# Optimization experiments

Hardware: AMD Instinct MI355X
Metric: run time of the kernel (lower is better)

## Reference

```python
import jax, jax.numpy as jnp
import numpy as np

BETA = 0.25


def setup_inputs() -> dict:
    key = jax.random.key(0)
    k1, k2 = jax.random.split(key)
    n_e, dim_e = 1024, 256
    z = jax.random.normal(k1, (32, dim_e, 32, 32), dtype=jnp.float32)
    # nn.Embedding init: uniform(-1/n_e, 1/n_e)
    embeddings = jax.random.uniform(k2, (n_e, dim_e), dtype=jnp.float32,
                                    minval=-1.0 / n_e, maxval=1.0 / n_e)
    return {"z": z, "embeddings": embeddings}


def reference(z, embeddings):
    B, C, H, W = z.shape
    # (B,C,H,W) -> (B*H*W, C)
    z_flat = jnp.transpose(z, (0, 2, 3, 1)).reshape(-1, C)
    # squared L2 distances to every codebook vector: (N, n_e)
    distances = (jnp.sum(z_flat ** 2, axis=1, keepdims=True)
                 + jnp.sum(embeddings ** 2, axis=1)
                 - 2.0 * z_flat @ embeddings.T)
    idx = jnp.argmin(distances, axis=1)  # (N,)
    # quantized vectors, back to (B,C,H,W)
    z_q = embeddings[idx].reshape(B, H, W, C).transpose(0, 3, 1, 2)
    sg = jax.lax.stop_gradient
    loss = (jnp.mean((sg(z_q) - z) ** 2)
            + BETA * jnp.mean((z_q - sg(z)) ** 2))
    # module returns the index map (B,H,W) and the scalar loss
    return idx.reshape(B, H, W), loss
```

## Files before the change

### kernel.cpp

```cpp
#include <hip/hip_runtime.h>


#define NE   1024
#define DIM  256
#define BHW  32768
#define CST  1024
#define BST  262144
#define NTH  256
#define MT   128
#define NT   128
#define KT   16
#define RT   8
#define CTY  8
#define ZSTR 160
#define NKT  (DIM / KT)
#define GAP_MFMA 1.5e-4f
#define GAP_F32  2.5e-4f

#define OFF_SUME   0
#define OFF_LOSS   4096
#define OFF_CNT    4112
#define OFF_T1     8192
#define OFF_BESTD  139264
#define OFF_LIST   270336
#define OFF_EMBT   401408
#define OFF_PART1  1449984
#define OFF_PART2  3547136
#define OFF_ZA     5242880
#define OFF_EB     38797312
#define WS_FAST_NEED 40894464ull

typedef unsigned long long ull;
typedef __attribute__((ext_vector_type(8))) short bf16x8;
typedef __attribute__((ext_vector_type(4))) float f32x4;

__device__ __forceinline__ unsigned short bf16rne(float x) {
    unsigned u = __float_as_uint(x);
    return (unsigned short)((u + 0x7fffu + ((u >> 16) & 1u)) >> 16);
}

__device__ __forceinline__ void gll16(const void* g, void* l) {
    __builtin_amdgcn_global_load_lds(
        (const __attribute__((address_space(1))) unsigned int*)g,
        (__attribute__((address_space(3))) unsigned int*)l, 16, 0, 0);
}

__device__ __forceinline__ float keyhi(ull k) {
    return __uint_as_float((unsigned)(k >> 32));
}
__device__ __forceinline__ void kmerge(ull& m1, float& m2, ull x1, float x2) {
    if (x1 < m1) { m2 = fminf(x2, keyhi(m1)); m1 = x1; }
    else          m2 = fminf(m2, keyhi(x1));
}

__device__ __forceinline__ float np_pw128_sq_contig(const float* p) {
    float r[8];
#pragma unroll
    for (int k = 0; k < 8; ++k) r[k] = __fmul_rn(p[k], p[k]);
    for (int i = 8; i < 128; i += 8) {
#pragma unroll
        for (int k = 0; k < 8; ++k)
            r[k] = __fadd_rn(r[k], __fmul_rn(p[i + k], p[i + k]));
    }
    return __fadd_rn(__fadd_rn(__fadd_rn(r[0], r[1]), __fadd_rn(r[2], r[3])),
                     __fadd_rn(__fadd_rn(r[4], r[5]), __fadd_rn(r[6], r[7])));
}

__global__ __launch_bounds__(NTH) void vq_prep(const float* __restrict__ emb,
                                               const float* __restrict__ z,
                                               float* __restrict__ sume,
                                               float* __restrict__ embT,
                                               unsigned short* __restrict__ Eb,
                                               unsigned short* __restrict__ Za,
                                               float* __restrict__ t1,
                                               double* __restrict__ loss_acc,
                                               int* __restrict__ cnt,
                                               int doEb) {
    __shared__ float zt[256 * 66];
    const int tid = threadIdx.x;

    if (blockIdx.x < 128) {
        if (blockIdx.x == 0 && tid == 0) { *loss_acc = 0.0; *cnt = 0; }
        const int j0   = blockIdx.x * 8;
        const int jloc = tid >> 5;
        const int c0   = (tid & 31) * 8;
        const int j    = j0 + jloc;

        const float4* gp = (const float4*)(emb + (size_t)j * DIM + c0);
        float4 v0 = gp[0], v1 = gp[1];
        float v[8] = {v0.x, v0.y, v0.z, v0.w, v1.x, v1.y, v1.z, v1.w};

#pragma unroll
        for (int k = 0; k < 8; ++k) zt[jloc * 264 + c0 + k] = v[k];

        if (doEb) {
            bf16x8 p1, p2;
#pragma unroll
            for (int k = 0; k < 8; ++k) {
                unsigned short b1 = bf16rne(v[k]);
                float b1f = __uint_as_float((unsigned)b1 << 16);
                unsigned short b2 = bf16rne(__fsub_rn(v[k], b1f));
                p1[k] = (short)b1;
                p2[k] = (short)b2;
            }
            const int kta = c0 >> 5, pos = c0 & 31;
            *(bf16x8*)(Eb + (size_t)kta * 32768 + (size_t)j * 32 + pos)       = p1;
            *(bf16x8*)(Eb + (size_t)(kta + 8) * 32768 + (size_t)j * 32 + pos) = p2;
        }
        __syncthreads();
        {
            float col[8];
#pragma unroll
            for (int r = 0; r < 8; ++r) col[r] = zt[r * 264 + tid];
            float4 w0 = {col[0], col[1], col[2], col[3]};
            float4 w1 = {col[4], col[5], col[6], col[7]};
            *(float4*)(embT + (size_t)tid * NE + j0)     = w0;
            *(float4*)(embT + (size_t)tid * NE + j0 + 4) = w1;
        }
        if (tid < 8) {
            const float* p = &zt[tid * 264];
            sume[j0 + tid] = __fadd_rn(np_pw128_sq_contig(p),
                                       np_pw128_sq_contig(p + 128));
        }
        return;
    }

    const int zb = blockIdx.x - 128;
    const int b = zb >> 4, hw0 = (zb & 15) * 64;
    const int idx = tid & 63, cq = tid >> 6;
    for (int c = cq * 64; c < cq * 64 + 64; ++c)
        zt[c * 66 + idx] = z[(size_t)b * BST + (size_t)c * CST + hw0 + idx];
    __syncthreads();
    if (tid < 64) {
        float r[8], h[2];
#pragma unroll
        for (int half = 0; half < 2; ++half) {
            int c0 = half * 128;
#pragma unroll
            for (int k = 0; k < 8; ++k) {
                float v = zt[(c0 + k) * 66 + tid];
                r[k] = __fmul_rn(v, v);
            }
            for (int c = 8; c < 128; ++c) {
                float v = zt[(c0 + c) * 66 + tid];
                r[c & 7] = __fadd_rn(r[c & 7], __fmul_rn(v, v));
            }
            h[half] = __fadd_rn(
                __fadd_rn(__fadd_rn(r[0], r[1]), __fadd_rn(r[2], r[3])),
                __fadd_rn(__fadd_rn(r[4], r[5]), __fadd_rn(r[6], r[7])));
        }
        t1[b * 1024 + hw0 + tid] = __fadd_rn(h[0], h[1]);
    }
    const int l = tid & 63, seg = tid >> 6;
    const int rloc = seg * 16 + (l >> 2), piece = l & 3;
    const int n = b * 1024 + hw0 + rloc;
    for (int kt = 0; kt < 16; ++kt) {
        bf16x8 pack;
        int cbase = (kt & 7) * 32 + piece * 8;
#pragma unroll
        for (int jj = 0; jj < 8; ++jj) {
            float zf = zt[(cbase + jj) * 66 + rloc];
            unsigned short a1 = bf16rne(zf);
            unsigned short v = a1;
            if (kt >= 8) {
                float a1f = __uint_as_float((unsigned)a1 << 16);
                v = bf16rne(__fsub_rn(zf, a1f));
            }
            pack[jj] = (short)v;
        }
        *(bf16x8*)(Za + (size_t)kt * 1048576 + (size_t)n * 32 + piece * 8) = pack;
    }
}

__global__ __launch_bounds__(NTH) void vq_mfma(const unsigned short* __restrict__ Za,
                                               const unsigned short* __restrict__ Eb,
                                               const float* __restrict__ sume,
                                               const float* __restrict__ t1g,
                                               ull* __restrict__ part1,
                                               float* __restrict__ part2) {
    __shared__ __align__(16) unsigned short As[8192];
    __shared__ __align__(16) unsigned short Bs[8192];
    __shared__ ull   red1[128];
    __shared__ float red2[128];

    const int tid = threadIdx.x;
    const int w = tid >> 6, lane = tid & 63;
    const int wr = w & 1, wc = w >> 1;
    const int c15 = lane & 15, q = lane >> 4;
    const int blk = blockIdx.x;
    const int ct = (blk >> 3) & 7;
    const int rowtile = ((blk >> 6) << 3) | (blk & 7);
    const int row0 = rowtile * MT;

    const int perm = (lane >> 2) * 32 + (((lane & 3) ^ ((lane >> 3) & 3)) * 8);
    const int qs = (q ^ ((c15 >> 1) & 3)) * 8;

    f32x4 acc[4][4];
#pragma unroll
    for (int i = 0; i < 4; ++i)
#pragma unroll
        for (int jb = 0; jb < 4; ++jb) acc[i][jb] = (f32x4){0.f, 0.f, 0.f, 0.f};

    const int s0 = w * 2;
    for (int ktp = 0; ktp < 8; ++ktp) {
        __syncthreads();
        {
            const unsigned short* gAlo = Za + (size_t)ktp * 1048576 + (size_t)row0 * 32;
            const unsigned short* gAhi = gAlo + 8u * 1048576u;
            const unsigned short* gBlo = Eb + (size_t)ktp * 32768 + (size_t)ct * 4096;
            const unsigned short* gBhi = gBlo + 8u * 32768u;
#pragma unroll
            for (int ss = 0; ss < 2; ++ss) {
                const int s = s0 + ss;
                gll16(gAlo + s * 512 + perm, (void*)&As[s * 512]);
                gll16(gAhi + s * 512 + perm, (void*)&As[4096 + s * 512]);
                gll16(gBlo + s * 512 + perm, (void*)&Bs[s * 512]);
                gll16(gBhi + s * 512 + perm, (void*)&Bs[4096 + s * 512]);
            }
        }
        __syncthreads();

        bf16x8 bl[4], bh[4];
#pragma unroll
        for (int jb = 0; jb < 4; ++jb) {
            const int nn = (wc * 64 + jb * 16 + c15) * 32 + qs;
            bl[jb] = *(const bf16x8*)&Bs[nn];
            bh[jb] = *(const bf16x8*)&Bs[4096 + nn];
        }
#pragma unroll
        for (int i = 0; i < 4; ++i) {
            const int mm = (wr * 64 + i * 16 + c15) * 32 + qs;
            bf16x8 al = *(const bf16x8*)&As[mm];
            bf16x8 ah = *(const bf16x8*)&As[4096 + mm];
#pragma unroll
            for (int jb = 0; jb < 4; ++jb) {
                acc[i][jb] = __builtin_amdgcn_mfma_f32_16x16x32_bf16(
                    al, bl[jb], acc[i][jb], 0, 0, 0);
                acc[i][jb] = __builtin_amdgcn_mfma_f32_16x16x32_bf16(
                    al, bh[jb], acc[i][jb], 0, 0, 0);
                acc[i][jb] = __builtin_amdgcn_mfma_f32_16x16x32_bf16(
                    ah, bl[jb], acc[i][jb], 0, 0, 0);
            }
        }
    }

    float sme[4];
#pragma unroll
    for (int jb = 0; jb < 4; ++jb)
        sme[jb] = sume[ct * 128 + wc * 64 + jb * 16 + c15];

    ull   mm1[4][4];
    float mm2[4][4];
#pragma unroll
    for (int i = 0; i < 4; ++i) {
#pragma unroll
        for (int reg = 0; reg < 4; ++reg) {
            int row = row0 + wr * 64 + i * 16 + q * 4 + reg;
            float t1v = t1g[row];
            ull m1 = ~0ull;
            float m2 = 3.4e38f;
#pragma unroll
            for (int jb = 0; jb < 4; ++jb) {
                float d = __fsub_rn(__fadd_rn(t1v, sme[jb]),
                                    __fmul_rn(2.0f, acc[i][jb][reg]));
                ull key = ((ull)__float_as_uint(d) << 32) |
                          (unsigned)(ct * 128 + wc * 64 + jb * 16 + c15);
                kmerge(m1, m2, key, 3.4e38f);
            }
#pragma unroll
            for (int m = 1; m < 16; m <<= 1) {
                ull x1 = __shfl_xor(m1, m);
                float x2 = __shfl_xor(m2, m);
                kmerge(m1, m2, x1, x2);
            }
            mm1[i][reg] = m1;
            mm2[i][reg] = m2;
        }
    }
    if (wc == 0 && c15 == 0) {
#pragma unroll
        for (int i = 0; i < 4; ++i)
#pragma unroll
            for (int reg = 0; reg < 4; ++reg) {
                red1[wr * 64 + i * 16 + q * 4 + reg] = mm1[i][reg];
                red2[wr * 64 + i * 16 + q * 4 + reg] = mm2[i][reg];
            }
    }
    __syncthreads();
    if (wc == 1 && c15 == 0) {
#pragma unroll
        for (int i = 0; i < 4; ++i)
#pragma unroll
            for (int reg = 0; reg < 4; ++reg) {
                int loc = wr * 64 + i * 16 + q * 4 + reg;
                ull m1 = mm1[i][reg];
                float m2 = mm2[i][reg];
                kmerge(m1, m2, red1[loc], red2[loc]);
                part1[(size_t)ct * BHW + row0 + loc] = m1;
                part2[(size_t)ct * BHW + row0 + loc] = m2;
            }
    }
}

__global__ __launch_bounds__(NTH) void vq_main_f32(const float* __restrict__ z,
                                                   const float* __restrict__ emb,
                                                   const float* __restrict__ sume,
                                                   const float* __restrict__ t1g,
                                                   ull* __restrict__ part1,
                                                   float* __restrict__ part2) {
    __shared__ __align__(16) char smem[25344];
    float* zs = (float*)smem;
    float* es = zs + KT * ZSTR;
    ull* red1 = (ull*)smem;
    float* red2 = (float*)(smem + 16896);

    const int tid = threadIdx.x;
    const int rowtile = blockIdx.x & 255;
    const int split = blockIdx.x >> 8;
    const int row0 = rowtile * MT;
    const int b = row0 >> 10;
    const int hw0 = row0 & 1023;
    const int rg = tid & 15, cg = tid >> 4;
    const int sm = tid & 127, skh = tid >> 7;
    const int sn = tid >> 1, skq = tid & 1;

    const float* zstg = z + (size_t)b * BST + hw0 + sm;
    const int zi = (sm >> 3) * 10 + (sm & 7);
    const int ei = (sn >> 3) * 10 + (sn & 7);

    float t1v[RT];
#pragma unroll
    for (int i = 0; i < RT; ++i) t1v[i] = t1g[row0 + rg * RT + i];

    ull b1[RT];
    float b2[RT];
#pragma unroll
    for (int i = 0; i < RT; ++i) { b1[i] = ~0ull; b2[i] = 3.4e38f; }

    const int code0 = split * NT;
    float accf[RT][CTY];
#pragma unroll
    for (int i = 0; i < RT; ++i)
#pragma unroll
        for (int j = 0; j < CTY; ++j) accf[i][j] = 0.0f;

    float smv[CTY];
#pragma unroll
    for (int j = 0; j < CTY; ++j) smv[j] = sume[code0 + cg * CTY + j];

    const float* estg = emb + (size_t)(code0 + sn) * DIM + skq * 8;

    for (int kt = 0; kt < NKT; ++kt) {
        __syncthreads();
        {
            const float* zp = zstg + (size_t)(kt * KT + skh) * CST;
#pragma unroll
            for (int kk = 0; kk < 8; ++kk)
                zs[(kk * 2 + skh) * ZSTR + zi] = zp[(size_t)(kk * 2) * CST];
        }
        {
            const float4* ep = (const float4*)(estg + kt * KT);
            float4 e0 = ep[0], e1 = ep[1];
            float ev[8] = {e0.x, e0.y, e0.z, e0.w, e1.x, e1.y, e1.z, e1.w};
#pragma unroll
            for (int qq = 0; qq < 8; ++qq)
                es[(skq * 8 + qq) * ZSTR + ei] = ev[qq];
        }
        __syncthreads();

#pragma unroll 2
        for (int k = 0; k < KT; ++k) {
            const float* zf = &zs[k * ZSTR + rg * 10];
            const float* ef = &es[k * ZSTR + cg * 10];
            float zr[RT], er[CTY];
#pragma unroll
            for (int i = 0; i < RT; ++i) zr[i] = zf[i];
#pragma unroll
            for (int j = 0; j < CTY; ++j) er[j] = ef[j];
#pragma unroll
            for (int i = 0; i < RT; ++i)
#pragma unroll
                for (int j = 0; j < CTY; ++j)
                    accf[i][j] = fmaf(zr[i], er[j], accf[i][j]);
        }
    }

#pragma unroll
    for (int i = 0; i < RT; ++i)
#pragma unroll
        for (int j = 0; j < CTY; ++j) {
            float d = __fsub_rn(__fadd_rn(t1v[i], smv[j]),
                                __fmul_rn(2.0f, accf[i][j]));
            ull key = ((ull)__float_as_uint(d) << 32) |
                      (unsigned)(code0 + cg * CTY + j);
            kmerge(b1[i], b2[i], key, 3.4e38f);
        }

    __syncthreads();
#pragma unroll
    for (int i = 0; i < RT; ++i) {
        red1[cg * 132 + rg * RT + i] = b1[i];
        red2[cg * 132 + rg * RT + i] = b2[i];
    }
    __syncthreads();
    if (tid < MT) {
        ull m1 = red1[tid];
        float m2 = red2[tid];
#pragma unroll
        for (int c = 1; c < 16; ++c)
            kmerge(m1, m2, red1[c * 132 + tid], red2[c * 132 + tid]);
        part1[(size_t)split * BHW + row0 + tid] = m1;
        part2[(size_t)split * BHW + row0 + tid] = m2;
    }
}

__global__ __launch_bounds__(NTH) void vq_t1(const float* __restrict__ z,
                                             float* __restrict__ t1) {
    int n = blockIdx.x * NTH + threadIdx.x;
    int b = n >> 10, hw = n & 1023;
    const float* p = z + (size_t)b * BST + hw;
    float r[8], h[2];
#pragma unroll
    for (int half = 0; half < 2; ++half) {
        int c0 = half * 128;
#pragma unroll
        for (int k = 0; k < 8; ++k) {
            float v = p[(size_t)(c0 + k) * CST];
            r[k] = __fmul_rn(v, v);
        }
        for (int c = 8; c < 128; ++c) {
            float v = p[(size_t)(c0 + c) * CST];
            r[c & 7] = __fadd_rn(r[c & 7], __fmul_rn(v, v));
        }
        h[half] = __fadd_rn(
            __fadd_rn(__fadd_rn(r[0], r[1]), __fadd_rn(r[2], r[3])),
            __fadd_rn(__fadd_rn(r[4], r[5]), __fadd_rn(r[6], r[7])));
    }
    t1[n] = __fadd_rn(h[0], h[1]);
}

__global__ __launch_bounds__(NTH) void vq_combine(const ull* __restrict__ part1,
                                                  const float* __restrict__ part2,
                                                  float* __restrict__ out,
                                                  float* __restrict__ bestd,
                                                  int* __restrict__ list,
                                                  int* __restrict__ cnt,
                                                  double* __restrict__ loss_acc,
                                                  float gapthr) {
    __shared__ double sdd[NTH];
    const int n = blockIdx.x * NTH + threadIdx.x;
    ull m1 = part1[n];
    float m2 = part2[n];
    for (int s = 1; s < 8; ++s)
        kmerge(m1, m2, part1[(size_t)s * BHW + n], part2[(size_t)s * BHW + n]);
    int j = (int)(m1 & 0xffffffffu);
    float d1 = keyhi(m1);
    out[n] = (float)j;
    bestd[n] = d1;
    float gap = __fsub_rn(m2, d1);
    if (!(gap >= gapthr)) {
        int p = atomicAdd(cnt, 1);
        list[p] = n;
    }
    sdd[threadIdx.x] = (double)d1;
    __syncthreads();
    for (int s = NTH / 2; s > 0; s >>= 1) {
        if (threadIdx.x < s) sdd[threadIdx.x] += sdd[threadIdx.x + s];
        __syncthreads();
    }
    if (threadIdx.x == 0) atomicAdd(loss_acc, sdd[0]);
}

__global__ __launch_bounds__(NTH) void vq_recheck(const float* __restrict__ z,
                                                  const float* __restrict__ embT,
                                                  const float* __restrict__ sume,
                                                  const float* __restrict__ t1g,
                                                  const int* __restrict__ list,
                                                  const int* __restrict__ cnt,
                                                  float* __restrict__ out,
                                                  const float* __restrict__ bestd,
                                                  double* __restrict__ loss_acc) {
    __shared__ float zs[DIM];
    __shared__ ull sk[NTH];
    const int t = threadIdx.x;
    int count = *cnt;
    if (count > BHW) count = BHW;
    const float4* ev = (const float4*)embT;

    for (int li = blockIdx.x; li < count; li += gridDim.x) {
        const int n = list[li];
        const int bb = n >> 10, hw = n & 1023;
        __syncthreads();
        zs[t] = z[(size_t)bb * BST + (size_t)t * CST + hw];
        __syncthreads();

        double acc[4] = {0.0, 0.0, 0.0, 0.0};
#pragma unroll 4
        for (int c = 0; c < DIM; ++c) {
            float4 e = ev[c * 256 + t];
            double zv = (double)zs[c];
            acc[0] = fma(zv, (double)e.x, acc[0]);
            acc[1] = fma(zv, (double)e.y, acc[1]);
            acc[2] = fma(zv, (double)e.z, acc[2]);
            acc[3] = fma(zv, (double)e.w, acc[3]);
        }
        const float t1v = t1g[n];
        const float4 sm = ((const float4*)sume)[t];
        const float smv[4] = {sm.x, sm.y, sm.z, sm.w};
        ull bk = ~0ull;
#pragma unroll
        for (int jj = 0; jj < 4; ++jj) {
            int j = t * 4 + jj;
            float d = __fsub_rn(__fadd_rn(t1v, smv[jj]),
                                __fmul_rn(2.0f, (float)acc[jj]));
            ull key = ((ull)__float_as_uint(d) << 32) | (unsigned)j;
            if (key < bk) bk = key;
        }
        sk[t] = bk;
        __syncthreads();
        for (int s = NTH / 2; s > 0; s >>= 1) {
            if (t < s) { ull o = sk[t + s]; if (o < sk[t]) sk[t] = o; }
            __syncthreads();
        }
        if (t == 0) {
            int j = (int)(sk[0] & 0xffffffffu);
            out[n] = (float)j;
            atomicAdd(loss_acc, (double)keyhi(sk[0]) - (double)bestd[n]);
        }
    }
}

__global__ void vq_final(const double* __restrict__ acc,
                         float* __restrict__ out) {
    double m = *acc / 8388608.0;
    float mf = (float)m;
    out[BHW] = __fadd_rn(mf, __fmul_rn(0.25f, mf));
}

extern "C" void kernel_launch(void* const* d_in, const int* in_sizes, int n_in,
                              void* d_out, int out_size, void* d_ws, size_t ws_size,
                              hipStream_t stream) {
    const float* z = (const float*)d_in[0];
    const float* emb = (const float*)d_in[1];
    float* out = (float*)d_out;

    char* ws = (char*)d_ws;
    float* sume = (float*)(ws + OFF_SUME);
    double* loss_acc = (double*)(ws + OFF_LOSS);
    int* cnt = (int*)(ws + OFF_CNT);
    float* t1 = (float*)(ws + OFF_T1);
    float* bestd = (float*)(ws + OFF_BESTD);
    int* list = (int*)(ws + OFF_LIST);
    float* embT = (float*)(ws + OFF_EMBT);
    ull* part1 = (ull*)(ws + OFF_PART1);
    float* part2 = (float*)(ws + OFF_PART2);
    unsigned short* Za = (unsigned short*)(ws + OFF_ZA);
    unsigned short* Eb = (unsigned short*)(ws + OFF_EB);

    const bool fast = ws_size >= WS_FAST_NEED;

    if (fast) {
        vq_prep<<<640, NTH, 0, stream>>>(emb, z, sume, embT, Eb, Za, t1,
                                         loss_acc, cnt, 1);
        vq_mfma<<<2048, NTH, 0, stream>>>(Za, Eb, sume, t1, part1, part2);
    } else {
        vq_prep<<<128, NTH, 0, stream>>>(emb, z, sume, embT, Eb, Za, t1,
                                         loss_acc, cnt, 0);
        vq_t1<<<BHW / NTH, NTH, 0, stream>>>(z, t1);
        vq_main_f32<<<2048, NTH, 0, stream>>>(z, emb, sume, t1, part1, part2);
    }
    vq_combine<<<BHW / NTH, NTH, 0, stream>>>(part1, part2, out, bestd, list, cnt,
                                              loss_acc, fast ? GAP_MFMA : GAP_F32);
    vq_recheck<<<2048, NTH, 0, stream>>>(z, embT, sume, t1, list, cnt, out, bestd,
                                         loss_acc);
    vq_final<<<1, 1, 0, stream>>>(loss_acc, out);
}
```

Baseline: 219.5 us.

## Fuse combine, recheck and final loss into one post kernel

Merges the partial-result combine, the fp64 recheck of near-tie rows and the final loss reduction into a single kernel. Each block keeps its ambiguous rows in a shared-memory list and rechecks them locally. A last-block-done counter then writes the scalar loss. This removes two kernel launches, the global candidate list and the bestd round-trip. The cost is that rechecks run serially within each of 128 blocks rather than across a 2048-block grid, which could create imbalance if many rows are ambiguous.

Measured after the change: 378.3 us. 1.72x slower.

```diff
diff --git a/kernel.cpp b/kernel.cpp
--- a/kernel.cpp
+++ b/kernel.cpp
@@ -19,10 +19,8 @@
 
 #define OFF_SUME   0
 #define OFF_LOSS   4096
-#define OFF_CNT    4112
+#define OFF_DONE   4112
 #define OFF_T1     8192
-#define OFF_BESTD  139264
-#define OFF_LIST   270336
 #define OFF_EMBT   401408
 #define OFF_PART1  1449984
 #define OFF_PART2  3547136
@@ -74,13 +72,13 @@
                                                unsigned short* __restrict__ Za,
                                                float* __restrict__ t1,
                                                double* __restrict__ loss_acc,
-                                               int* __restrict__ cnt,
+                                               int* __restrict__ done,
                                                int doEb) {
     __shared__ float zt[256 * 66];
     const int tid = threadIdx.x;
 
     if (blockIdx.x < 128) {
-        if (blockIdx.x == 0 && tid == 0) { *loss_acc = 0.0; *cnt = 0; }
+        if (blockIdx.x == 0 && tid == 0) { *loss_acc = 0.0; *done = 0; }
         const int j0   = blockIdx.x * 8;
         const int jloc = tid >> 5;
         const int c0   = (tid & 31) * 8;
@@ -439,57 +437,57 @@
     t1[n] = __fadd_rn(h[0], h[1]);
 }
 
-__global__ __launch_bounds__(NTH) void vq_combine(const ull* __restrict__ part1,
-                                                  const float* __restrict__ part2,
-                                                  float* __restrict__ out,
-                                                  float* __restrict__ bestd,
-                                                  int* __restrict__ list,
-                                                  int* __restrict__ cnt,
-                                                  double* __restrict__ loss_acc,
-                                                  float gapthr) {
+__global__ __launch_bounds__(NTH) void vq_post(const ull* __restrict__ part1,
+                                               const float* __restrict__ part2,
+                                               const float* __restrict__ z,
+                                               const float* __restrict__ embT,
+                                               const float* __restrict__ sume,
+                                               const float* __restrict__ t1g,
+                                               float* __restrict__ out,
+                                               double* __restrict__ loss_acc,
+                                               int* __restrict__ done,
+                                               float gapthr) {
     __shared__ double sdd[NTH];
-    const int n = blockIdx.x * NTH + threadIdx.x;
+    __shared__ float  zs[DIM];
+    __shared__ ull    sk[NTH];
+    __shared__ int    lrows[NTH];
+    __shared__ float  ld1[NTH];
+    __shared__ int    lcnt;
+    __shared__ double blockloss;
+
+    const int t = threadIdx.x;
+    const int n = blockIdx.x * NTH + t;
+    if (t == 0) lcnt = 0;
+    __syncthreads();
+
     ull m1 = part1[n];
     float m2 = part2[n];
     for (int s = 1; s < 8; ++s)
         kmerge(m1, m2, part1[(size_t)s * BHW + n], part2[(size_t)s * BHW + n]);
-    int j = (int)(m1 & 0xffffffffu);
-    float d1 = keyhi(m1);
-    out[n] = (float)j;
-    bestd[n] = d1;
+    const int jwin = (int)(m1 & 0xffffffffu);
+    const float d1 = keyhi(m1);
+    out[n] = (float)jwin;
     float gap = __fsub_rn(m2, d1);
     if (!(gap >= gapthr)) {
-        int p = atomicAdd(cnt, 1);
-        list[p] = n;
-    }
-    sdd[threadIdx.x] = (double)d1;
+        int p = atomicAdd(&lcnt, 1);
+        lrows[p] = n;
+        ld1[p] = d1;
+    }
+    sdd[t] = (double)d1;
     __syncthreads();
     for (int s = NTH / 2; s > 0; s >>= 1) {
-        if (threadIdx.x < s) sdd[threadIdx.x] += sdd[threadIdx.x + s];
-        __syncthreads();
-    }
-    if (threadIdx.x == 0) atomicAdd(loss_acc, sdd[0]);
-}
-
-__global__ __launch_bounds__(NTH) void vq_recheck(const float* __restrict__ z,
-                                                  const float* __restrict__ embT,
-                                                  const float* __restrict__ sume,
-                                                  const float* __restrict__ t1g,
-                                                  const int* __restrict__ list,
-                                                  const int* __restrict__ cnt,
-                                                  float* __restrict__ out,
-                                                  const float* __restrict__ bestd,
-                                                  double* __restrict__ loss_acc) {
-    __shared__ float zs[DIM];
-    __shared__ ull sk[NTH];
-    const int t = threadIdx.x;
-    int count = *cnt;
-    if (count > BHW) count = BHW;
+        if (t < s) sdd[t] += sdd[t + s];
+        __syncthreads();
+    }
+    if (t == 0) blockloss = sdd[0];
+    const int count = lcnt;
+
     const float4* ev = (const float4*)embT;
-
-    for (int li = blockIdx.x; li < count; li += gridDim.x) {
-        const int n = list[li];
-        const int bb = n >> 10, hw = n & 1023;
+    const float4 smq = ((const float4*)sume)[t];
+    const float smv[4] = {smq.x, smq.y, smq.z, smq.w};
+    for (int li = 0; li < count; ++li) {
+        const int nr = lrows[li];
+        const int bb = nr >> 10, hw = nr & 1023;
         __syncthreads();
         zs[t] = z[(size_t)bb * BST + (size_t)t * CST + hw];
         __syncthreads();
@@ -504,9 +502,7 @@
             acc[2] = fma(zv, (double)e.z, acc[2]);
             acc[3] = fma(zv, (double)e.w, acc[3]);
         }
-        const float t1v = t1g[n];
-        const float4 sm = ((const float4*)sume)[t];
-        const float smv[4] = {sm.x, sm.y, sm.z, sm.w};
+        const float t1v = t1g[nr];
         ull bk = ~0ull;
 #pragma unroll
         for (int jj = 0; jj < 4; ++jj) {
@@ -524,17 +520,24 @@
         }
         if (t == 0) {
             int j = (int)(sk[0] & 0xffffffffu);
-            out[n] = (float)j;
-            atomicAdd(loss_acc, (double)keyhi(sk[0]) - (double)bestd[n]);
-        }
-    }
-}
-
-__global__ void vq_final(const double* __restrict__ acc,
-                         float* __restrict__ out) {
-    double m = *acc / 8388608.0;
-    float mf = (float)m;
-    out[BHW] = __fadd_rn(mf, __fmul_rn(0.25f, mf));
+            out[nr] = (float)j;
+            blockloss += (double)keyhi(sk[0]) - (double)ld1[li];
+        }
+    }
+    __syncthreads();
+
+    if (t == 0) {
+        atomicAdd(loss_acc, blockloss);
+        __threadfence();
+        int o = atomicAdd(done, 1);
+        if (o == (int)gridDim.x - 1) {
+            __threadfence();
+            double total = atomicAdd(loss_acc, 0.0);
+            double m = total / 8388608.0;
+            float mf = (float)m;
+            out[BHW] = __fadd_rn(mf, __fmul_rn(0.25f, mf));
+        }
+    }
 }
 
 extern "C" void kernel_launch(void* const* d_in, const int* in_sizes, int n_in,
@@ -547,10 +550,8 @@
     char* ws = (char*)d_ws;
     float* sume = (float*)(ws + OFF_SUME);
     double* loss_acc = (double*)(ws + OFF_LOSS);
-    int* cnt = (int*)(ws + OFF_CNT);
+    int* done = (int*)(ws + OFF_DONE);
     float* t1 = (float*)(ws + OFF_T1);
-    float* bestd = (float*)(ws + OFF_BESTD);
-    int* list = (int*)(ws + OFF_LIST);
     float* embT = (float*)(ws + OFF_EMBT);
     ull* part1 = (ull*)(ws + OFF_PART1);
     float* part2 = (float*)(ws + OFF_PART2);
@@ -561,17 +562,15 @@
 
     if (fast) {
         vq_prep<<<640, NTH, 0, stream>>>(emb, z, sume, embT, Eb, Za, t1,
-                                         loss_acc, cnt, 1);
+                                         loss_acc, done, 1);
         vq_mfma<<<2048, NTH, 0, stream>>>(Za, Eb, sume, t1, part1, part2);
     } else {
         vq_prep<<<128, NTH, 0, stream>>>(emb, z, sume, embT, Eb, Za, t1,
-                                         loss_acc, cnt, 0);
+                                         loss_acc, done, 0);
         vq_t1<<<BHW / NTH, NTH, 0, stream>>>(z, t1);
         vq_main_f32<<<2048, NTH, 0, stream>>>(z, emb, sume, t1, part1, part2);
     }
-    vq_combine<<<BHW / NTH, NTH, 0, stream>>>(part1, part2, out, bestd, list, cnt,
-                                              loss_acc, fast ? GAP_MFMA : GAP_F32);
-    vq_recheck<<<2048, NTH, 0, stream>>>(z, embT, sume, t1, list, cnt, out, bestd,
-                                         loss_acc);
-    vq_final<<<1, 1, 0, stream>>>(loss_acc, out);
-}
+    vq_post<<<BHW / NTH, NTH, 0, stream>>>(part1, part2, z, embT, sume, t1,
+                                           out, loss_acc, done,
+                                           fast ? GAP_MFMA : GAP_F32);
+}
```
